# Kernel optimization log

Hardware: AMD Instinct MI355X
Metric: run time of the kernel (lower is better)

Reference implementation:

```python
import jax, jax.numpy as jnp
import numpy as np

B, Himg, Wimg, C, HID, R = 16, 64, 64, 256, 512, 2
CLIP = 3.0
NULL_LOGIT = 0.0
WARMUP_ETA = 1.0


def _ln(x, g, b, eps=1e-5):
    m = x.mean(-1, keepdims=True)
    v = ((x - m) ** 2).mean(-1, keepdims=True)
    return (x - m) * jax.lax.rsqrt(v + eps) * g + b


def _mlp(x, W1, b1, W2, b2):
    # Linear -> GELU (erf, torch default) -> Linear
    return jax.nn.gelu(x @ W1 + b1, approximate=False) @ W2 + b2


def setup_inputs() -> dict:
    key = jax.random.key(0)
    ks = jax.random.split(key, 8)
    s = 0.02
    return {
        "states": jax.random.normal(ks[0], (B, Himg * Wimg, C), jnp.float32),
        "ln_c_g": jnp.ones((C,), jnp.float32),
        "ln_c_b": jnp.zeros((C,), jnp.float32),
        "parent_seed": jax.random.normal(ks[1], (1, 1, C), jnp.float32) * s,
        "dW1": jax.random.normal(ks[2], (3 * C, HID), jnp.float32) * s,
        "db1": jnp.zeros((HID,), jnp.float32),
        "dW2": jax.random.normal(ks[3], (HID, 1), jnp.float32) * s,
        "db2": jnp.zeros((1,), jnp.float32),
        "rW1": jax.random.normal(ks[4], (3 * C, HID), jnp.float32) * s,
        "rb1": jnp.zeros((HID,), jnp.float32),
        "rW2": jax.random.normal(ks[5], (HID, 1), jnp.float32) * s,
        "rb2": jnp.zeros((1,), jnp.float32),
        "vW": jax.random.normal(ks[6], (C, C), jnp.float32) * s,
        "vb": jnp.zeros((C,), jnp.float32),
        "e_bias": jnp.full((1,), -0.1, jnp.float32),
        "ln_o_g": jnp.ones((C,), jnp.float32),
        "ln_o_b": jnp.zeros((C,), jnp.float32),
        "image_h": Himg,
        "image_w": Wimg,
    }


def reference(states, ln_c_g, ln_c_b, parent_seed, dW1, db1, dW2, db2,
              rW1, rb1, rW2, rb2, vW, vb, e_bias, ln_o_g, ln_o_b,
              image_h, image_w):
    b = states.shape[0]
    ph, pw = image_h // R, image_w // R
    # [B,H,W,C] -> [B, ph*pw, R*R, C] local 2x2 child groups
    grid = states.reshape(b, image_h, image_w, C)
    groups = grid.reshape(b, ph, R, pw, R, C).transpose(0, 1, 3, 2, 4, 5)
    groups = groups.reshape(b, ph * pw, R * R, C)

    normalized = _ln(groups, ln_c_g, ln_c_b)            # child LayerNorm
    gm = normalized.mean(axis=2, keepdims=True)          # group mean (mask all-true)
    gm_b = jnp.broadcast_to(gm, normalized.shape)
    joint = jnp.concatenate([normalized, gm_b, normalized * gm_b], axis=-1)

    drive = _mlp(joint, dW1, db1, dW2, db2)              # [B,P,G,1]
    variance = ((normalized - gm) ** 2).mean(-1, keepdims=True)
    resistance = jax.nn.softplus(_mlp(joint, rW1, rb1, rW2, rb2)) + variance

    # EMLUnit: clipped drive/resistance energy with learned bias
    energy = jnp.clip(WARMUP_ETA * drive / (resistance + 1e-6) + e_bias,
                      -CLIP, CLIP)[..., 0]               # [B,P,G]

    # EMLResponsibility: null-aware softmax over children + null slot
    null = jnp.full(energy.shape[:-1] + (1,), NULL_LOGIT, energy.dtype)
    probs = jax.nn.softmax(jnp.concatenate([energy, null], axis=-1), axis=-1)
    weights = probs[..., :-1]                            # neighbor_weights [B,P,G]
    null_weight = probs[..., -1:]                        # [B,P,1]
    update_strength = 1.0 - null_weight                  # [B,P,1]

    values = normalized @ vW + vb                        # value_proj
    candidate = jnp.einsum('bpg,bpgc->bpc', weights, values)

    # EMLPrecisionUpdate with old_confidence=0: blend seed toward candidate
    old_state = parent_seed                              # broadcasts over [B,P,C]
    new_state = old_state + update_strength * (candidate - old_state)
    parent_state = _ln(new_state, ln_o_g, ln_o_b)
    return parent_state
```

## Files before the change

### kernel.cpp

```cpp
#include <hip/hip_runtime.h>
#include <hip/hip_bf16.h>
#include <math.h>

#define BATCH 16
#define PGRID 1024
#define NGRP  (BATCH*PGRID)
#define NELEM (NGRP*4)
#define CDIM  256
#define HID   512

#define OFF_N     ((size_t)0)
#define OFF_GM    ((size_t)16777216)
#define OFF_VAR   ((size_t)20971520)
#define OFF_DRIVE ((size_t)21037056)
#define OFF_RPRE  ((size_t)21102592)
#define OFF_WN    ((size_t)21168128)
#define OFF_US    ((size_t)25362432)
#define OFF_W1TH  ((size_t)25378816)
#define OFF_W1TL  ((size_t)25772032)

__device__ __forceinline__ unsigned short f2bf(float x) {
  unsigned u = __float_as_uint(x);
  unsigned r = u + 0x7FFFu + ((u >> 16) & 1u);
  return (unsigned short)(r >> 16);
}
__device__ __forceinline__ float bf2f(unsigned short h) {
  return __uint_as_float(((unsigned)h) << 16);
}

__device__ __forceinline__ void wave_reduce4(float v[4]) {
#pragma unroll
  for (int off = 1; off < 64; off <<= 1) {
#pragma unroll
    for (int i = 0; i < 4; ++i) v[i] += __shfl_xor(v[i], off, 64);
  }
}

__device__ __forceinline__ void block_reduce4(float v[4], float* sh ) {
  wave_reduce4(v);
  const int lane = threadIdx.x & 63, wid = threadIdx.x >> 6;
  __syncthreads();
  if (lane == 0) {
#pragma unroll
    for (int i = 0; i < 4; ++i) sh[wid * 4 + i] = v[i];
  }
  __syncthreads();
#pragma unroll
  for (int i = 0; i < 4; ++i) v[i] = sh[i] + sh[4 + i] + sh[8 + i] + sh[12 + i];
}

__global__ __launch_bounds__(256) void prep_kernel(
    const float* __restrict__ states,
    const float* __restrict__ ln_c_g, const float* __restrict__ ln_c_b,
    float* __restrict__ nbuf, float* __restrict__ gmbuf, float* __restrict__ varb,
    float* __restrict__ drive, float* __restrict__ rpre)
{
  __shared__ float sh[16];
  const int g = blockIdx.x;
  const int b = g >> 10;
  const int p = g & 1023;
  const int py = p >> 5, px = p & 31;
  const int c = threadIdx.x;

  float x[4];
#pragma unroll
  for (int s = 0; s < 4; ++s) {
    const int h = py * 2 + (s >> 1);
    const int w = px * 2 + (s & 1);
    x[s] = states[((size_t)(b * 4096 + h * 64 + w)) * CDIM + c];
  }

  float sum[4] = {x[0], x[1], x[2], x[3]};
  block_reduce4(sum, sh);
  float d[4];
#pragma unroll
  for (int s = 0; s < 4; ++s) d[s] = x[s] - sum[s] * (1.f / 256.f);

  float sq[4] = {d[0]*d[0], d[1]*d[1], d[2]*d[2], d[3]*d[3]};
  block_reduce4(sq, sh);

  const float gg = ln_c_g[c], bb = ln_c_b[c];
  float nn[4];
#pragma unroll
  for (int s = 0; s < 4; ++s)
    nn[s] = d[s] * rsqrtf(sq[s] * (1.f / 256.f) + 1e-5f) * gg + bb;

  const float gmc = 0.25f * (nn[0] + nn[1] + nn[2] + nn[3]);
  float e4[4];
#pragma unroll
  for (int s = 0; s < 4; ++s) { const float t = nn[s] - gmc; e4[s] = t * t; }
  block_reduce4(e4, sh);

  const size_t nb = (size_t)g * 4 * CDIM;
#pragma unroll
  for (int s = 0; s < 4; ++s) nbuf[nb + s * CDIM + c] = nn[s];
  gmbuf[(size_t)g * CDIM + c] = gmc;
  if (c < 4) {
    varb[g * 4 + c] = e4[c] * (1.f / 256.f);
    drive[g * 4 + c] = 0.f;
    rpre[g * 4 + c] = 0.f;
  }
}

__global__ __launch_bounds__(256) void prew1_kernel(
    const float* __restrict__ dW1, const float* __restrict__ rW1,
    short* __restrict__ w1th, short* __restrict__ w1tl)
{
  const int col = blockIdx.x;
  const float* W1 = (col < 512) ? dW1 : rW1;
  const int cl = (col < 512) ? col : col - 512;
  for (int k = threadIdx.x; k < 768; k += 256) {
    const float x = W1[(size_t)k * HID + cl];
    const unsigned short h = f2bf(x);
    const unsigned short l = f2bf(x - bf2f(h));
    w1th[(size_t)col * 768 + k] = (short)h;
    w1tl[(size_t)col * 768 + k] = (short)l;
  }
}

typedef __attribute__((ext_vector_type(8))) short  frag_ab;
typedef __attribute__((ext_vector_type(4))) float  frag_cd;

#define LDS_STRIDE 40

__global__ __launch_bounds__(256) void mlp_gemm_mfma(
    const float* __restrict__ nbuf, const float* __restrict__ gmbuf,
    const short* __restrict__ w1th, const short* __restrict__ w1tl,
    const float* __restrict__ db1, const float* __restrict__ rb1,
    const float* __restrict__ dW2, const float* __restrict__ rW2,
    float* __restrict__ drive, float* __restrict__ rpre)
{
  __shared__ __align__(16) short Ah[128 * LDS_STRIDE];
  __shared__ __align__(16) short Al[128 * LDS_STRIDE];
  __shared__ __align__(16) short Bh[128 * LDS_STRIDE];
  __shared__ __align__(16) short Bl[128 * LDS_STRIDE];

  const int tid  = threadIdx.x;
  const int lane = tid & 63;
  const int w    = tid >> 6;
  const int wm   = w >> 1;
  const int wn   = w & 1;
  const int m_base = blockIdx.x * 128;
  const int n_base = blockIdx.y * 128;

  const int ar = tid >> 1;
  const int ac = (tid & 1) * 16;
  const int e  = m_base + ar;
  const float* nrow = nbuf + (size_t)e * CDIM;
  const float* grow = gmbuf + (size_t)(e >> 2) * CDIM;

  const int bcol = tid >> 1;
  const int bk   = (tid & 1) * 16;
  const short* bsrc_h = w1th + (size_t)(n_base + bcol) * 768 + bk;
  const short* bsrc_l = w1tl + (size_t)(n_base + bcol) * 768 + bk;

  frag_cd acc[4][4];
#pragma unroll
  for (int i = 0; i < 4; ++i)
#pragma unroll
    for (int j = 0; j < 4; ++j)
#pragma unroll
      for (int q = 0; q < 4; ++q) acc[i][j][q] = 0.f;

  float va[16];
  float4 vbh0, vbh1, vbl0, vbl1;

#define LOADA(K0) {                                                         \
    const int kb = (K0) & 255;                                              \
    if ((K0) < 256) {                                                       \
      _Pragma("unroll")                                                     \
      for (int q = 0; q < 4; ++q) {                                         \
        const float4 t = *(const float4*)(nrow + kb + ac + q * 4);          \
        va[q*4+0] = t.x; va[q*4+1] = t.y; va[q*4+2] = t.z; va[q*4+3] = t.w; \
      }                                                                     \
    } else if ((K0) < 512) {                                                \
      _Pragma("unroll")                                                     \
      for (int q = 0; q < 4; ++q) {                                         \
        const float4 t = *(const float4*)(grow + kb + ac + q * 4);          \
        va[q*4+0] = t.x; va[q*4+1] = t.y; va[q*4+2] = t.z; va[q*4+3] = t.w; \
      }                                                                     \
    } else {                                                                \
      _Pragma("unroll")                                                     \
      for (int q = 0; q < 4; ++q) {                                         \
        const float4 t = *(const float4*)(nrow + kb + ac + q * 4);          \
        const float4 u = *(const float4*)(grow + kb + ac + q * 4);          \
        va[q*4+0] = t.x*u.x; va[q*4+1] = t.y*u.y;                           \
        va[q*4+2] = t.z*u.z; va[q*4+3] = t.w*u.w;                           \
      }                                                                     \
    }                                                                       \
  }

#define LOADB(K0) {                                                         \
    const float4* ph = (const float4*)(bsrc_h + (K0));                      \
    vbh0 = ph[0]; vbh1 = ph[1];                                             \
    const float4* pl = (const float4*)(bsrc_l + (K0));                      \
    vbl0 = pl[0]; vbl1 = pl[1];                                             \
  }

  LOADA(0); LOADB(0);

  for (int kk = 0; kk < 24; ++kk) {
    __syncthreads();
    frag_ab ph0, ph1, pl0, pl1;
#pragma unroll
    for (int i = 0; i < 8; ++i) {
      const unsigned short h = f2bf(va[i]);
      const unsigned short l = f2bf(va[i] - bf2f(h));
      ph0[i] = (short)h; pl0[i] = (short)l;
    }
#pragma unroll
    for (int i = 0; i < 8; ++i) {
      const unsigned short h = f2bf(va[8 + i]);
      const unsigned short l = f2bf(va[8 + i] - bf2f(h));
      ph1[i] = (short)h; pl1[i] = (short)l;
    }
    *(frag_ab*)&Ah[ar * LDS_STRIDE + ac]     = ph0;
    *(frag_ab*)&Ah[ar * LDS_STRIDE + ac + 8] = ph1;
    *(frag_ab*)&Al[ar * LDS_STRIDE + ac]     = pl0;
    *(frag_ab*)&Al[ar * LDS_STRIDE + ac + 8] = pl1;
    *(float4*)&Bh[bcol * LDS_STRIDE + bk]     = vbh0;
    *(float4*)&Bh[bcol * LDS_STRIDE + bk + 8] = vbh1;
    *(float4*)&Bl[bcol * LDS_STRIDE + bk]     = vbl0;
    *(float4*)&Bl[bcol * LDS_STRIDE + bk + 8] = vbl1;
    __syncthreads();

    if (kk < 23) { const int k0 = (kk + 1) * 32; LOADA(k0); LOADB(k0); }

    const int kq = 8 * (lane >> 4);
    frag_ab bhf[4], blf[4];
#pragma unroll
    for (int nf = 0; nf < 4; ++nf) {
      const int cb = (wn * 64 + nf * 16 + (lane & 15)) * LDS_STRIDE + kq;
      bhf[nf] = *(frag_ab*)&Bh[cb];
      blf[nf] = *(frag_ab*)&Bl[cb];
    }
#pragma unroll
    for (int mf = 0; mf < 4; ++mf) {
      const int rb = (wm * 64 + mf * 16 + (lane & 15)) * LDS_STRIDE + kq;
      const frag_ab ahf = *(frag_ab*)&Ah[rb];
      const frag_ab alf = *(frag_ab*)&Al[rb];
#pragma unroll
      for (int nf = 0; nf < 4; ++nf) {
        acc[mf][nf] = __builtin_amdgcn_mfma_f32_16x16x32_bf16(ahf, bhf[nf], acc[mf][nf], 0, 0, 0);
        acc[mf][nf] = __builtin_amdgcn_mfma_f32_16x16x32_bf16(ahf, blf[nf], acc[mf][nf], 0, 0, 0);
        acc[mf][nf] = __builtin_amdgcn_mfma_f32_16x16x32_bf16(alf, bhf[nf], acc[mf][nf], 0, 0, 0);
      }
    }
  }

  const bool is_d = (n_base < 512);
  const float* b1v = is_d ? db1 : rb1;
  const float* W2v = is_d ? dW2 : rW2;
  float* tgt = is_d ? drive : rpre;
  const int joff = n_base - (is_d ? 0 : 512) + wn * 64;

  float part[4][4];
#pragma unroll
  for (int i = 0; i < 4; ++i)
#pragma unroll
    for (int q = 0; q < 4; ++q) part[i][q] = 0.f;

#pragma unroll
  for (int nf = 0; nf < 4; ++nf) {
    const int j = joff + nf * 16 + (lane & 15);
    const float bb = b1v[j];
    const float ww = W2v[j];
#pragma unroll
    for (int mf = 0; mf < 4; ++mf)
#pragma unroll
      for (int q = 0; q < 4; ++q) {
        const float xv = acc[mf][nf][q] + bb;
        const float ge = 0.5f * xv * (1.f + erff(xv * 0.70710678118654752f));
        part[mf][q] = fmaf(ge, ww, part[mf][q]);
      }
  }
#pragma unroll
  for (int off = 1; off < 16; off <<= 1)
#pragma unroll
    for (int mf = 0; mf < 4; ++mf)
#pragma unroll
      for (int q = 0; q < 4; ++q)
        part[mf][q] += __shfl_xor(part[mf][q], off, 64);

  if ((lane & 15) == 0) {
    const int rq = lane >> 4;
#pragma unroll
    for (int mf = 0; mf < 4; ++mf)
#pragma unroll
      for (int q = 0; q < 4; ++q)
        atomicAdd(&tgt[m_base + wm * 64 + mf * 16 + rq * 4 + q], part[mf][q]);
  }
}

__global__ __launch_bounds__(256) void weights_kernel(
    const float* __restrict__ nbuf, const float* __restrict__ drive,
    const float* __restrict__ rpre, const float* __restrict__ varb,
    const float* __restrict__ db2, const float* __restrict__ rb2,
    const float* __restrict__ e_bias,
    float* __restrict__ wn, float* __restrict__ usb)
{
  const int g = blockIdx.x;
  const int c = threadIdx.x;
  const float eb = e_bias[0];
  const float b2d = db2[0], b2r = rb2[0];

  float w[4];
  float mx = 0.f;
#pragma unroll
  for (int s = 0; s < 4; ++s) {
    const float dr = drive[g * 4 + s] + b2d;
    const float rp = rpre[g * 4 + s] + b2r;
    const float va = varb[g * 4 + s];
    const float sp = fmaxf(rp, 0.f) + log1pf(expf(-fabsf(rp)));
    float en = dr / (sp + va + 1e-6f) + eb;
    en = fminf(3.f, fmaxf(-3.f, en));
    w[s] = en;
    mx = fmaxf(mx, en);
  }
  const float nullw = expf(-mx);
  float Z = nullw;
#pragma unroll
  for (int s = 0; s < 4; ++s) { w[s] = expf(w[s] - mx); Z += w[s]; }
  const float inv = 1.f / Z;

  float a = 0.f;
  const size_t nb = (size_t)g * 4 * CDIM;
#pragma unroll
  for (int s = 0; s < 4; ++s) a = fmaf(w[s] * inv, nbuf[nb + s * CDIM + c], a);
  wn[(size_t)g * CDIM + c] = a;
  if (c == 0) usb[g] = 1.f - nullw * inv;
}

__global__ __launch_bounds__(256) void final_kernel(
    const float* __restrict__ wn, const float* __restrict__ usb,
    const float* __restrict__ vW, const float* __restrict__ vb,
    const float* __restrict__ seed,
    const float* __restrict__ ln_o_g, const float* __restrict__ ln_o_b,
    float* __restrict__ out)
{
  __shared__ float lwn[16][256];
  const int t = threadIdx.x;
  const int g0 = blockIdx.x * 16;
#pragma unroll
  for (int gi = 0; gi < 16; ++gi)
    lwn[gi][t] = wn[(size_t)(g0 + gi) * CDIM + t];
  __syncthreads();

  const int cq = (t & 63) * 4;
  const int gq = (t >> 6) * 4;

  float acc[4][4];
#pragma unroll
  for (int gi = 0; gi < 4; ++gi)
#pragma unroll
    for (int j = 0; j < 4; ++j) acc[gi][j] = 0.f;

  for (int k = 0; k < 256; ++k) {
    const float4 w4 = *(const float4*)(vW + (size_t)k * CDIM + cq);
#pragma unroll
    for (int gi = 0; gi < 4; ++gi) {
      const float a = lwn[gq + gi][k];
      acc[gi][0] = fmaf(a, w4.x, acc[gi][0]);
      acc[gi][1] = fmaf(a, w4.y, acc[gi][1]);
      acc[gi][2] = fmaf(a, w4.z, acc[gi][2]);
      acc[gi][3] = fmaf(a, w4.w, acc[gi][3]);
    }
  }

  const float4 sd  = *(const float4*)(seed + cq);
  const float4 og  = *(const float4*)(ln_o_g + cq);
  const float4 ob  = *(const float4*)(ln_o_b + cq);
  const float4 vb4 = *(const float4*)(vb + cq);

#pragma unroll
  for (int gi = 0; gi < 4; ++gi) {
    const float us = usb[g0 + gq + gi];
    float nv[4];
    nv[0] = sd.x + us * (acc[gi][0] + us * vb4.x - sd.x);
    nv[1] = sd.y + us * (acc[gi][1] + us * vb4.y - sd.y);
    nv[2] = sd.z + us * (acc[gi][2] + us * vb4.z - sd.z);
    nv[3] = sd.w + us * (acc[gi][3] + us * vb4.w - sd.w);

    float s = nv[0] + nv[1] + nv[2] + nv[3];
#pragma unroll
    for (int off = 1; off < 64; off <<= 1) s += __shfl_xor(s, off, 64);
    const float m = s * (1.f / 256.f);

    const float d0 = nv[0] - m, d1 = nv[1] - m, d2 = nv[2] - m, d3 = nv[3] - m;
    float q = d0 * d0 + d1 * d1 + d2 * d2 + d3 * d3;
#pragma unroll
    for (int off = 1; off < 64; off <<= 1) q += __shfl_xor(q, off, 64);
    const float rstd = rsqrtf(q * (1.f / 256.f) + 1e-5f);

    float4 o;
    o.x = d0 * rstd * og.x + ob.x;
    o.y = d1 * rstd * og.y + ob.y;
    o.z = d2 * rstd * og.z + ob.z;
    o.w = d3 * rstd * og.w + ob.w;
    *(float4*)(out + (size_t)(g0 + gq + gi) * CDIM + cq) = o;
  }
}

extern "C" void kernel_launch(void* const* d_in, const int* in_sizes, int n_in,
                              void* d_out, int out_size, void* d_ws, size_t ws_size,
                              hipStream_t stream)
{
  const float* states = (const float*)d_in[0];
  const float* ln_c_g = (const float*)d_in[1];
  const float* ln_c_b = (const float*)d_in[2];
  const float* seed   = (const float*)d_in[3];
  const float* dW1    = (const float*)d_in[4];
  const float* db1    = (const float*)d_in[5];
  const float* dW2    = (const float*)d_in[6];
  const float* db2    = (const float*)d_in[7];
  const float* rW1    = (const float*)d_in[8];
  const float* rb1    = (const float*)d_in[9];
  const float* rW2    = (const float*)d_in[10];
  const float* rb2    = (const float*)d_in[11];
  const float* vW     = (const float*)d_in[12];
  const float* vb     = (const float*)d_in[13];
  const float* e_bias = (const float*)d_in[14];
  const float* ln_o_g = (const float*)d_in[15];
  const float* ln_o_b = (const float*)d_in[16];
  float* out = (float*)d_out;

  float* ws    = (float*)d_ws;
  float* nbuf  = ws + OFF_N;
  float* gmbuf = ws + OFF_GM;
  float* varb  = ws + OFF_VAR;
  float* drive = ws + OFF_DRIVE;
  float* rpre  = ws + OFF_RPRE;
  float* wnb   = ws + OFF_WN;
  float* usb   = ws + OFF_US;
  short* w1th  = (short*)(ws + OFF_W1TH);
  short* w1tl  = (short*)(ws + OFF_W1TL);

  prep_kernel<<<NGRP, 256, 0, stream>>>(states, ln_c_g, ln_c_b,
                                        nbuf, gmbuf, varb, drive, rpre);

  prew1_kernel<<<1024, 256, 0, stream>>>(dW1, rW1, w1th, w1tl);

  dim3 ggrid(512, 8);
  mlp_gemm_mfma<<<ggrid, 256, 0, stream>>>(nbuf, gmbuf, w1th, w1tl,
                                           db1, rb1, dW2, rW2, drive, rpre);

  weights_kernel<<<NGRP, 256, 0, stream>>>(nbuf, drive, rpre, varb,
                                           db2, rb2, e_bias, wnb, usb);

  final_kernel<<<NGRP / 16, 256, 0, stream>>>(wnb, usb, vW, vb, seed,
                                              ln_o_g, ln_o_b, out);
}
```

Measured before the change: 852.2 us.

## Store normalized activations as bf16 hi/lo pairs and remap GEMM tiles per XCD

The prep kernel now writes the normalized children and group means as pre-split bf16 high/low halves instead of fp32, so the GEMM can copy A fragments straight into LDS for two-thirds of the K range and only re-split the product section. The LDS tiles switch from a padded row-major layout to a sectioned layout indexed by k-chunk. The 2D grid becomes a 1D grid remapped so each XCD handles a contiguous band of M tiles across all N tiles, which should improve L2 reuse of A. The weights kernel reconstructs values from hi+lo; precision is preserved, but the product section now reconstructs inputs and re-splits them, adding some ALU work.

New measurement: 842.9 us. About the same (-1.1%).

```diff
diff --git a/kernel.cpp b/kernel.cpp
--- a/kernel.cpp
+++ b/kernel.cpp
@@ -9,8 +9,10 @@
 #define CDIM  256
 #define HID   512
 
-#define OFF_N     ((size_t)0)
-#define OFF_GM    ((size_t)16777216)
+#define OFF_NH    ((size_t)0)
+#define OFF_NL    ((size_t)8388608)
+#define OFF_GMH   ((size_t)16777216)
+#define OFF_GML   ((size_t)18874368)
 #define OFF_VAR   ((size_t)20971520)
 #define OFF_DRIVE ((size_t)21037056)
 #define OFF_RPRE  ((size_t)21102592)
@@ -52,8 +54,9 @@
 __global__ __launch_bounds__(256) void prep_kernel(
     const float* __restrict__ states,
     const float* __restrict__ ln_c_g, const float* __restrict__ ln_c_b,
-    float* __restrict__ nbuf, float* __restrict__ gmbuf, float* __restrict__ varb,
-    float* __restrict__ drive, float* __restrict__ rpre)
+    short* __restrict__ nh, short* __restrict__ nl,
+    short* __restrict__ gmh, short* __restrict__ gml,
+    float* __restrict__ varb, float* __restrict__ drive, float* __restrict__ rpre)
 {
   __shared__ float sh[16];
   const int g = blockIdx.x;
@@ -93,8 +96,18 @@
 
   const size_t nb = (size_t)g * 4 * CDIM;
 #pragma unroll
-  for (int s = 0; s < 4; ++s) nbuf[nb + s * CDIM + c] = nn[s];
-  gmbuf[(size_t)g * CDIM + c] = gmc;
+  for (int s = 0; s < 4; ++s) {
+    const unsigned short h = f2bf(nn[s]);
+    const unsigned short l = f2bf(nn[s] - bf2f(h));
+    nh[nb + s * CDIM + c] = (short)h;
+    nl[nb + s * CDIM + c] = (short)l;
+  }
+  {
+    const unsigned short h = f2bf(gmc);
+    const unsigned short l = f2bf(gmc - bf2f(h));
+    gmh[(size_t)g * CDIM + c] = (short)h;
+    gml[(size_t)g * CDIM + c] = (short)l;
+  }
   if (c < 4) {
     varb[g * 4 + c] = e4[c] * (1.f / 256.f);
     drive[g * 4 + c] = 0.f;
@@ -121,36 +134,47 @@
 typedef __attribute__((ext_vector_type(8))) short  frag_ab;
 typedef __attribute__((ext_vector_type(4))) float  frag_cd;
 
-#define LDS_STRIDE 40
+#define AIDX(sec, row) ((sec) * 1024 + (row) * 8)
 
 __global__ __launch_bounds__(256) void mlp_gemm_mfma(
-    const float* __restrict__ nbuf, const float* __restrict__ gmbuf,
+    const short* __restrict__ nh, const short* __restrict__ nl,
+    const short* __restrict__ gmh, const short* __restrict__ gml,
     const short* __restrict__ w1th, const short* __restrict__ w1tl,
     const float* __restrict__ db1, const float* __restrict__ rb1,
     const float* __restrict__ dW2, const float* __restrict__ rW2,
     float* __restrict__ drive, float* __restrict__ rpre)
 {
-  __shared__ __align__(16) short Ah[128 * LDS_STRIDE];
-  __shared__ __align__(16) short Al[128 * LDS_STRIDE];
-  __shared__ __align__(16) short Bh[128 * LDS_STRIDE];
-  __shared__ __align__(16) short Bl[128 * LDS_STRIDE];
+  __shared__ __align__(16) short Ah[4096];
+  __shared__ __align__(16) short Al[4096];
+  __shared__ __align__(16) short Bh[4096];
+  __shared__ __align__(16) short Bl[4096];
 
   const int tid  = threadIdx.x;
   const int lane = tid & 63;
   const int w    = tid >> 6;
   const int wm   = w >> 1;
   const int wn   = w & 1;
-  const int m_base = blockIdx.x * 128;
-  const int n_base = blockIdx.y * 128;
+
+  const int bid = blockIdx.x;
+  const int xcd = bid & 7;
+  const int lb  = bid >> 3;
+  const int mt  = xcd * 64 + (lb >> 3);
+  const int nt  = lb & 7;
+  const int m_base = mt * 128;
+  const int n_base = nt * 128;
 
   const int ar = tid >> 1;
   const int ac = (tid & 1) * 16;
+  const int asec = (tid & 1) * 2;
   const int e  = m_base + ar;
-  const float* nrow = nbuf + (size_t)e * CDIM;
-  const float* grow = gmbuf + (size_t)(e >> 2) * CDIM;
+  const short* nhrow = nh + (size_t)e * CDIM;
+  const short* nlrow = nl + (size_t)e * CDIM;
+  const short* ghrow = gmh + (size_t)(e >> 2) * CDIM;
+  const short* glrow = gml + (size_t)(e >> 2) * CDIM;
 
   const int bcol = tid >> 1;
   const int bk   = (tid & 1) * 16;
+  const int bsec = (tid & 1) * 2;
   const short* bsrc_h = w1th + (size_t)(n_base + bcol) * 768 + bk;
   const short* bsrc_l = w1tl + (size_t)(n_base + bcol) * 768 + bk;
 
@@ -162,83 +186,101 @@
 #pragma unroll
       for (int q = 0; q < 4; ++q) acc[i][j][q] = 0.f;
 
+  frag_ab sA0, sA1, sA2, sA3;
   float va[16];
-  float4 vbh0, vbh1, vbl0, vbl1;
-
-#define LOADA(K0) {                                                         \
-    const int kb = (K0) & 255;                                              \
-    if ((K0) < 256) {                                                       \
-      _Pragma("unroll")                                                     \
-      for (int q = 0; q < 4; ++q) {                                         \
-        const float4 t = *(const float4*)(nrow + kb + ac + q * 4);          \
-        va[q*4+0] = t.x; va[q*4+1] = t.y; va[q*4+2] = t.z; va[q*4+3] = t.w; \
-      }                                                                     \
-    } else if ((K0) < 512) {                                                \
-      _Pragma("unroll")                                                     \
-      for (int q = 0; q < 4; ++q) {                                         \
-        const float4 t = *(const float4*)(grow + kb + ac + q * 4);          \
-        va[q*4+0] = t.x; va[q*4+1] = t.y; va[q*4+2] = t.z; va[q*4+3] = t.w; \
-      }                                                                     \
-    } else {                                                                \
-      _Pragma("unroll")                                                     \
-      for (int q = 0; q < 4; ++q) {                                         \
-        const float4 t = *(const float4*)(nrow + kb + ac + q * 4);          \
-        const float4 u = *(const float4*)(grow + kb + ac + q * 4);          \
-        va[q*4+0] = t.x*u.x; va[q*4+1] = t.y*u.y;                           \
-        va[q*4+2] = t.z*u.z; va[q*4+3] = t.w*u.w;                           \
-      }                                                                     \
-    }                                                                       \
-  }
-
-#define LOADB(K0) {                                                         \
-    const float4* ph = (const float4*)(bsrc_h + (K0));                      \
-    vbh0 = ph[0]; vbh1 = ph[1];                                             \
-    const float4* pl = (const float4*)(bsrc_l + (K0));                      \
-    vbl0 = pl[0]; vbl1 = pl[1];                                             \
+  frag_ab sB0, sB1, sB2, sB3;
+
+#define LOADA(K0) {                                                          \
+    if ((K0) < 256) {                                                        \
+      sA0 = *(const frag_ab*)(nhrow + (K0) + ac);                            \
+      sA1 = *(const frag_ab*)(nhrow + (K0) + ac + 8);                        \
+      sA2 = *(const frag_ab*)(nlrow + (K0) + ac);                            \
+      sA3 = *(const frag_ab*)(nlrow + (K0) + ac + 8);                        \
+    } else if ((K0) < 512) {                                                 \
+      const int kb_ = (K0) - 256;                                            \
+      sA0 = *(const frag_ab*)(ghrow + kb_ + ac);                             \
+      sA1 = *(const frag_ab*)(ghrow + kb_ + ac + 8);                         \
+      sA2 = *(const frag_ab*)(glrow + kb_ + ac);                             \
+      sA3 = *(const frag_ab*)(glrow + kb_ + ac + 8);                         \
+    } else {                                                                 \
+      const int kb_ = (K0) - 512;                                            \
+      const frag_ab h0 = *(const frag_ab*)(nhrow + kb_ + ac);                \
+      const frag_ab h1 = *(const frag_ab*)(nhrow + kb_ + ac + 8);            \
+      const frag_ab l0 = *(const frag_ab*)(nlrow + kb_ + ac);                \
+      const frag_ab l1 = *(const frag_ab*)(nlrow + kb_ + ac + 8);            \
+      const frag_ab g0 = *(const frag_ab*)(ghrow + kb_ + ac);                \
+      const frag_ab g1 = *(const frag_ab*)(ghrow + kb_ + ac + 8);            \
+      const frag_ab m0 = *(const frag_ab*)(glrow + kb_ + ac);                \
+      const frag_ab m1 = *(const frag_ab*)(glrow + kb_ + ac + 8);            \
+      _Pragma("unroll")                                                      \
+      for (int i_ = 0; i_ < 8; ++i_) {                                       \
+        const float nf = bf2f((unsigned short)h0[i_]) + bf2f((unsigned short)l0[i_]); \
+        const float gf = bf2f((unsigned short)g0[i_]) + bf2f((unsigned short)m0[i_]); \
+        va[i_] = nf * gf;                                                    \
+      }                                                                      \
+      _Pragma("unroll")                                                      \
+      for (int i_ = 0; i_ < 8; ++i_) {                                       \
+        const float nf = bf2f((unsigned short)h1[i_]) + bf2f((unsigned short)l1[i_]); \
+        const float gf = bf2f((unsigned short)g1[i_]) + bf2f((unsigned short)m1[i_]); \
+        va[8 + i_] = nf * gf;                                                \
+      }                                                                      \
+    }                                                                        \
+  }
+
+#define LOADB(K0) {                                                          \
+    sB0 = *(const frag_ab*)(bsrc_h + (K0));                                  \
+    sB1 = *(const frag_ab*)(bsrc_h + (K0) + 8);                              \
+    sB2 = *(const frag_ab*)(bsrc_l + (K0));                                  \
+    sB3 = *(const frag_ab*)(bsrc_l + (K0) + 8);                              \
   }
 
   LOADA(0); LOADB(0);
 
   for (int kk = 0; kk < 24; ++kk) {
     __syncthreads();
-    frag_ab ph0, ph1, pl0, pl1;
-#pragma unroll
-    for (int i = 0; i < 8; ++i) {
-      const unsigned short h = f2bf(va[i]);
-      const unsigned short l = f2bf(va[i] - bf2f(h));
-      ph0[i] = (short)h; pl0[i] = (short)l;
+    if (kk < 16) {
+      *(frag_ab*)&Ah[AIDX(asec,     ar)] = sA0;
+      *(frag_ab*)&Ah[AIDX(asec + 1, ar)] = sA1;
+      *(frag_ab*)&Al[AIDX(asec,     ar)] = sA2;
+      *(frag_ab*)&Al[AIDX(asec + 1, ar)] = sA3;
+    } else {
+      frag_ab ph0, ph1, pl0, pl1;
+#pragma unroll
+      for (int i = 0; i < 8; ++i) {
+        const unsigned short h = f2bf(va[i]);
+        ph0[i] = (short)h; pl0[i] = (short)f2bf(va[i] - bf2f(h));
+      }
+#pragma unroll
+      for (int i = 0; i < 8; ++i) {
+        const unsigned short h = f2bf(va[8 + i]);
+        ph1[i] = (short)h; pl1[i] = (short)f2bf(va[8 + i] - bf2f(h));
+      }
+      *(frag_ab*)&Ah[AIDX(asec,     ar)] = ph0;
+      *(frag_ab*)&Ah[AIDX(asec + 1, ar)] = ph1;
+      *(frag_ab*)&Al[AIDX(asec,     ar)] = pl0;
+      *(frag_ab*)&Al[AIDX(asec + 1, ar)] = pl1;
     }
-#pragma unroll
-    for (int i = 0; i < 8; ++i) {
-      const unsigned short h = f2bf(va[8 + i]);
-      const unsigned short l = f2bf(va[8 + i] - bf2f(h));
-      ph1[i] = (short)h; pl1[i] = (short)l;
+    *(frag_ab*)&Bh[AIDX(bsec,     bcol)] = sB0;
+    *(frag_ab*)&Bh[AIDX(bsec + 1, bcol)] = sB1;
+    *(frag_ab*)&Bl[AIDX(bsec,     bcol)] = sB2;
+    *(frag_ab*)&Bl[AIDX(bsec + 1, bcol)] = sB3;
+    __syncthreads();
+
+    if (kk < 23) { const int k0 = (kk + 1) * 32; LOADA(k0); LOADB(k0); }
+
+    const int sec = lane >> 4;
+    frag_ab bhf[4], blf[4];
+#pragma unroll
+    for (int nf = 0; nf < 4; ++nf) {
+      const int cb = AIDX(sec, wn * 64 + nf * 16 + (lane & 15));
+      bhf[nf] = *(const frag_ab*)&Bh[cb];
+      blf[nf] = *(const frag_ab*)&Bl[cb];
     }
-    *(frag_ab*)&Ah[ar * LDS_STRIDE + ac]     = ph0;
-    *(frag_ab*)&Ah[ar * LDS_STRIDE + ac + 8] = ph1;
-    *(frag_ab*)&Al[ar * LDS_STRIDE + ac]     = pl0;
-    *(frag_ab*)&Al[ar * LDS_STRIDE + ac + 8] = pl1;
-    *(float4*)&Bh[bcol * LDS_STRIDE + bk]     = vbh0;
-    *(float4*)&Bh[bcol * LDS_STRIDE + bk + 8] = vbh1;
-    *(float4*)&Bl[bcol * LDS_STRIDE + bk]     = vbl0;
-    *(float4*)&Bl[bcol * LDS_STRIDE + bk + 8] = vbl1;
-    __syncthreads();
-
-    if (kk < 23) { const int k0 = (kk + 1) * 32; LOADA(k0); LOADB(k0); }
-
-    const int kq = 8 * (lane >> 4);
-    frag_ab bhf[4], blf[4];
-#pragma unroll
-    for (int nf = 0; nf < 4; ++nf) {
-      const int cb = (wn * 64 + nf * 16 + (lane & 15)) * LDS_STRIDE + kq;
-      bhf[nf] = *(frag_ab*)&Bh[cb];
-      blf[nf] = *(frag_ab*)&Bl[cb];
-    }
 #pragma unroll
     for (int mf = 0; mf < 4; ++mf) {
-      const int rb = (wm * 64 + mf * 16 + (lane & 15)) * LDS_STRIDE + kq;
-      const frag_ab ahf = *(frag_ab*)&Ah[rb];
-      const frag_ab alf = *(frag_ab*)&Al[rb];
+      const int rb = AIDX(sec, wm * 64 + mf * 16 + (lane & 15));
+      const frag_ab ahf = *(const frag_ab*)&Ah[rb];
+      const frag_ab alf = *(const frag_ab*)&Al[rb];
 #pragma unroll
       for (int nf = 0; nf < 4; ++nf) {
         acc[mf][nf] = __builtin_amdgcn_mfma_f32_16x16x32_bf16(ahf, bhf[nf], acc[mf][nf], 0, 0, 0);
@@ -293,8 +335,9 @@
 }
 
 __global__ __launch_bounds__(256) void weights_kernel(
-    const float* __restrict__ nbuf, const float* __restrict__ drive,
-    const float* __restrict__ rpre, const float* __restrict__ varb,
+    const short* __restrict__ nh, const short* __restrict__ nl,
+    const float* __restrict__ drive, const float* __restrict__ rpre,
+    const float* __restrict__ varb,
     const float* __restrict__ db2, const float* __restrict__ rb2,
     const float* __restrict__ e_bias,
     float* __restrict__ wn, float* __restrict__ usb)
@@ -326,7 +369,11 @@
   float a = 0.f;
   const size_t nb = (size_t)g * 4 * CDIM;
 #pragma unroll
-  for (int s = 0; s < 4; ++s) a = fmaf(w[s] * inv, nbuf[nb + s * CDIM + c], a);
+  for (int s = 0; s < 4; ++s) {
+    const size_t ix = nb + s * CDIM + c;
+    const float nv = bf2f((unsigned short)nh[ix]) + bf2f((unsigned short)nl[ix]);
+    a = fmaf(w[s] * inv, nv, a);
+  }
   wn[(size_t)g * CDIM + c] = a;
   if (c == 0) usb[g] = 1.f - nullw * inv;
 }
@@ -425,8 +472,10 @@
   float* out = (float*)d_out;
 
   float* ws    = (float*)d_ws;
-  float* nbuf  = ws + OFF_N;
-  float* gmbuf = ws + OFF_GM;
+  short* nhb   = (short*)(ws + OFF_NH);
+  short* nlb   = (short*)(ws + OFF_NL);
+  short* gmhb  = (short*)(ws + OFF_GMH);
+  short* gmlb  = (short*)(ws + OFF_GML);
   float* varb  = ws + OFF_VAR;
   float* drive = ws + OFF_DRIVE;
   float* rpre  = ws + OFF_RPRE;
@@ -436,15 +485,14 @@
   short* w1tl  = (short*)(ws + OFF_W1TL);
 
   prep_kernel<<<NGRP, 256, 0, stream>>>(states, ln_c_g, ln_c_b,
-                                        nbuf, gmbuf, varb, drive, rpre);
+                                        nhb, nlb, gmhb, gmlb, varb, drive, rpre);
 
   prew1_kernel<<<1024, 256, 0, stream>>>(dW1, rW1, w1th, w1tl);
 
-  dim3 ggrid(512, 8);
-  mlp_gemm_mfma<<<ggrid, 256, 0, stream>>>(nbuf, gmbuf, w1th, w1tl,
-                                           db1, rb1, dW2, rW2, drive, rpre);
-
-  weights_kernel<<<NGRP, 256, 0, stream>>>(nbuf, drive, rpre, varb,
+  mlp_gemm_mfma<<<4096, 256, 0, stream>>>(nhb, nlb, gmhb, gmlb, w1th, w1tl,
+                                          db1, rb1, dW2, rW2, drive, rpre);
+
+  weights_kernel<<<NGRP, 256, 0, stream>>>(nhb, nlb, drive, rpre, varb,
                                            db2, rb2, e_bias, wnb, usb);
 
   final_kernel<<<NGRP / 16, 256, 0, stream>>>(wnb, usb, vW, vb, seed,
```
